# Kernel optimization log

Measured on AMD Instinct MI355X. Metric: run time of the kernel, lower is better.

Reference implementation:

```python
import jax, jax.numpy as jnp
import numpy as np

B, L = 64, 2048
N_RESTYPE, N_GROUP, N_ATOM = 21, 8, 14


def _compose(R1, t1, R2, t2):
    # rigid compose: (R1,t1) o (R2,t2) = (R1@R2, R1@t2 + t1)
    R = jnp.einsum('...ij,...jk->...ik', R1, R2)
    t = jnp.einsum('...ij,...j->...i', R1, t2) + t1
    return R, t


def setup_inputs() -> dict:
    key = jax.random.key(0)
    ks = jax.random.split(key, 8)
    return {
        'bb_rots': jax.random.normal(ks[0], (B, L, 3, 3), jnp.float32),
        'bb_trans': jax.random.normal(ks[1], (B, L, 3), jnp.float32),
        'angles': jax.random.normal(ks[2], (B, L, 7, 2), jnp.float32),
        'aatype': jax.random.randint(ks[3], (B, L), 0, N_RESTYPE),
        'default_frames': jax.random.normal(ks[4], (N_RESTYPE, N_GROUP, 4, 4), jnp.float32),
        'group_idx': jax.random.randint(ks[5], (N_RESTYPE, N_ATOM), 0, N_GROUP),
        'atom_mask': jax.random.uniform(ks[6], (N_RESTYPE, N_ATOM), jnp.float32),
        'lit_positions': jax.random.normal(ks[7], (N_RESTYPE, N_ATOM, 3), jnp.float32),
    }


def reference(bb_rots, bb_trans, angles, aatype, default_frames, group_idx, atom_mask, lit_positions):
    # ---- torsion_angles_to_frames ----
    d4 = default_frames[aatype]                      # [B,L,8,4,4]
    dR, dt = d4[..., :3, :3], d4[..., :3, 3]
    # prepend identity backbone torsion (sin=0, cos=1)
    bb = jnp.broadcast_to(jnp.array([0.0, 1.0], angles.dtype), (*angles.shape[:-2], 1, 2))
    ang = jnp.concatenate([bb, angles], axis=-2)     # [B,L,8,2]
    s, c = ang[..., 0], ang[..., 1]
    z, o = jnp.zeros_like(s), jnp.ones_like(s)
    # rotation about x-axis built from (sin, cos)
    rotx = jnp.stack([
        jnp.stack([o, z, z], axis=-1),
        jnp.stack([z, c, -s], axis=-1),
        jnp.stack([z, s, c], axis=-1),
    ], axis=-2)                                      # [B,L,8,3,3]
    fR = jnp.einsum('blgij,blgjk->blgik', dR, rotx)  # default_r.compose(all_rots)
    ft = dt                                          # all_rots has zero translation
    # chain chi2..chi4 onto chi1
    R5, t5 = _compose(fR[:, :, 4], ft[:, :, 4], fR[:, :, 5], ft[:, :, 5])
    R6, t6 = _compose(R5, t5, fR[:, :, 6], ft[:, :, 6])
    R7, t7 = _compose(R6, t6, fR[:, :, 7], ft[:, :, 7])
    Rbb = jnp.concatenate([fR[:, :, :5], R5[:, :, None], R6[:, :, None], R7[:, :, None]], axis=2)
    tbb = jnp.concatenate([ft[:, :, :5], t5[:, :, None], t6[:, :, None], t7[:, :, None]], axis=2)
    # compose with global backbone frame
    Rg = jnp.einsum('blij,blgjk->blgik', bb_rots, Rbb)          # [B,L,8,3,3]
    tg = jnp.einsum('blij,blgj->blgi', bb_rots, tbb) + bb_trans[:, :, None]

    # ---- frames_and_literature_positions_to_atom14_pos ----
    gidx = group_idx[aatype]                                    # [B,L,14]
    Ra = jnp.take_along_axis(Rg, gidx[:, :, :, None, None], axis=2)  # [B,L,14,3,3]
    ta = jnp.take_along_axis(tg, gidx[:, :, :, None], axis=2)        # [B,L,14,3]
    lit = lit_positions[aatype]                                 # [B,L,14,3]
    mask = atom_mask[aatype][..., None]                         # [B,L,14,1]
    pred = jnp.einsum('blaij,blaj->blai', Ra, lit) + ta
    return pred * mask
```

## Files before the change

kernel.cpp:

```cpp
#include <hip/hip_runtime.h>


constexpr int NRES_TOTAL = 64 * 2048;
constexpr int NRT = 21;
constexpr int NG  = 8;
constexpr int NA  = 14;

__global__ __launch_bounds__(256) void protein_mapper_kernel(
    const float* __restrict__ bb_rots,
    const float* __restrict__ bb_trans,
    const float* __restrict__ angles,
    const int*   __restrict__ aatype,
    const float* __restrict__ default_frames,
    const int*   __restrict__ group_idx,
    const float* __restrict__ atom_mask,
    const float* __restrict__ lit_positions,
    float* __restrict__ out)
{
    __shared__ float s_frames[NRT * NG * 16];
    __shared__ int   s_gidx[NRT * NA];
    __shared__ float s_mask[NRT * NA];
    __shared__ float s_lit[NRT * NA * 3];

    for (int j = threadIdx.x; j < NRT * NG * 16; j += 256) s_frames[j] = default_frames[j];
    for (int j = threadIdx.x; j < NRT * NA; j += 256) {
        s_gidx[j] = group_idx[j];
        s_mask[j] = atom_mask[j];
    }
    for (int j = threadIdx.x; j < NRT * NA * 3; j += 256) s_lit[j] = lit_positions[j];
    __syncthreads();

    const int i = blockIdx.x * 256 + threadIdx.x;
    if (i >= NRES_TOTAL) return;

    const int aa = aatype[i];

    float sv[NG], cv[NG];
    sv[0] = 0.0f; cv[0] = 1.0f;
    const float2* angp = reinterpret_cast<const float2*>(angles + (size_t)i * 14);
    #pragma unroll
    for (int g = 1; g < NG; ++g) {
        float2 sc = angp[g - 1];
        sv[g] = sc.x;
        cv[g] = sc.y;
    }

    float R[NG][9], t[NG][3];
    const float* fr = s_frames + aa * (NG * 16);
    #pragma unroll
    for (int g = 0; g < NG; ++g) {
        const float* m = fr + g * 16;
        const float cg = cv[g], sg = sv[g];
        #pragma unroll
        for (int r = 0; r < 3; ++r) {
            const float a0 = m[r * 4 + 0], a1 = m[r * 4 + 1], a2 = m[r * 4 + 2];
            R[g][r * 3 + 0] = a0;
            R[g][r * 3 + 1] = cg * a1 + sg * a2;
            R[g][r * 3 + 2] = cg * a2 - sg * a1;
            t[g][r] = m[r * 4 + 3];
        }
    }

    #pragma unroll
    for (int g = 5; g < NG; ++g) {
        float Q[9], tq[3];
        #pragma unroll
        for (int r = 0; r < 3; ++r) {
            const float p0 = R[g - 1][r * 3 + 0];
            const float p1 = R[g - 1][r * 3 + 1];
            const float p2 = R[g - 1][r * 3 + 2];
            #pragma unroll
            for (int cdx = 0; cdx < 3; ++cdx)
                Q[r * 3 + cdx] = p0 * R[g][cdx] + p1 * R[g][3 + cdx] + p2 * R[g][6 + cdx];
            tq[r] = p0 * t[g][0] + p1 * t[g][1] + p2 * t[g][2] + t[g - 1][r];
        }
        #pragma unroll
        for (int k = 0; k < 9; ++k) R[g][k] = Q[k];
        t[g][0] = tq[0]; t[g][1] = tq[1]; t[g][2] = tq[2];
    }

    const float* br = bb_rots + (size_t)i * 9;
    const float b00 = br[0], b01 = br[1], b02 = br[2];
    const float b10 = br[3], b11 = br[4], b12 = br[5];
    const float b20 = br[6], b21 = br[7], b22 = br[8];
    const float* btp = bb_trans + (size_t)i * 3;
    const float bt0 = btp[0], bt1 = btp[1], bt2 = btp[2];

    int   ga[NA];
    float mk[NA];
    #pragma unroll
    for (int a = 0; a < NA; ++a) {
        ga[a] = s_gidx[aa * NA + a];
        mk[a] = s_mask[aa * NA + a];
    }

    float res[NA * 3];
    #pragma unroll
    for (int g = 0; g < NG; ++g) {
        #pragma unroll
        for (int a = 0; a < NA; ++a) {
            if (ga[a] == g) {
                const float lx = s_lit[(aa * NA + a) * 3 + 0];
                const float ly = s_lit[(aa * NA + a) * 3 + 1];
                const float lz = s_lit[(aa * NA + a) * 3 + 2];
                const float px = R[g][0] * lx + R[g][1] * ly + R[g][2] * lz + t[g][0];
                const float py = R[g][3] * lx + R[g][4] * ly + R[g][5] * lz + t[g][1];
                const float pz = R[g][6] * lx + R[g][7] * ly + R[g][8] * lz + t[g][2];
                const float qx = b00 * px + b01 * py + b02 * pz + bt0;
                const float qy = b10 * px + b11 * py + b12 * pz + bt1;
                const float qz = b20 * px + b21 * py + b22 * pz + bt2;
                const float m_ = mk[a];
                res[a * 3 + 0] = qx * m_;
                res[a * 3 + 1] = qy * m_;
                res[a * 3 + 2] = qz * m_;
            }
        }
    }

    float2* op2 = reinterpret_cast<float2*>(out + (size_t)i * (NA * 3));
    #pragma unroll
    for (int k = 0; k < (NA * 3) / 2; ++k) {
        float2 v;
        v.x = res[2 * k + 0];
        v.y = res[2 * k + 1];
        op2[k] = v;
    }
}

extern "C" void kernel_launch(void* const* d_in, const int* in_sizes, int n_in,
                              void* d_out, int out_size, void* d_ws, size_t ws_size,
                              hipStream_t stream) {
    const float* bb_rots        = (const float*)d_in[0];
    const float* bb_trans       = (const float*)d_in[1];
    const float* angles         = (const float*)d_in[2];
    const int*   aatype         = (const int*)d_in[3];
    const float* default_frames = (const float*)d_in[4];
    const int*   group_idx      = (const int*)d_in[5];
    const float* atom_mask      = (const float*)d_in[6];
    const float* lit_positions  = (const float*)d_in[7];
    float* out = (float*)d_out;

    const int blocks = (NRES_TOTAL + 255) / 256;
    protein_mapper_kernel<<<blocks, 256, 0, stream>>>(
        bb_rots, bb_trans, angles, aatype,
        default_frames, group_idx, atom_mask, lit_positions, out);
}
```

Baseline: 108.2 us.

## Transpose shared tables by restype and select group frames with branchless muxes

Shared-memory lookup tables are stored transposed (element-major, restype-minor) so that threads with different aatype hit different LDS banks instead of strided rows. The per-atom group selection is replaced by a 3-level binary select tree over the 8 frames, so each atom is computed once instead of through a predicated 8x14 loop. Results are streamed directly into float2 stores per atom pair without a res array. This trades extra select instructions per atom for fewer divergent predicated blocks and less register pressure.

Result: faster. 93.46 us (-13.6%).

```diff
diff --git a/kernel.cpp b/kernel.cpp
--- a/kernel.cpp
+++ b/kernel.cpp
@@ -17,17 +17,24 @@
     const float* __restrict__ lit_positions,
     float* __restrict__ out)
 {
-    __shared__ float s_frames[NRT * NG * 16];
-    __shared__ int   s_gidx[NRT * NA];
-    __shared__ float s_mask[NRT * NA];
-    __shared__ float s_lit[NRT * NA * 3];
+    __shared__ float s_frames[128 * NRT];
+    __shared__ int   s_gidx[NA * NRT];
+    __shared__ float s_mask[NA * NRT];
+    __shared__ float s_lit[NA * 3 * NRT];
 
-    for (int j = threadIdx.x; j < NRT * NG * 16; j += 256) s_frames[j] = default_frames[j];
-    for (int j = threadIdx.x; j < NRT * NA; j += 256) {
-        s_gidx[j] = group_idx[j];
-        s_mask[j] = atom_mask[j];
+    for (int n = threadIdx.x; n < NRT * 128; n += 256) {
+        const int aa = n / 128, j = n % 128;
+        s_frames[j * NRT + aa] = default_frames[n];
     }
-    for (int j = threadIdx.x; j < NRT * NA * 3; j += 256) s_lit[j] = lit_positions[j];
+    for (int n = threadIdx.x; n < NRT * NA; n += 256) {
+        const int aa = n / NA, a = n % NA;
+        s_gidx[a * NRT + aa] = group_idx[n];
+        s_mask[a * NRT + aa] = atom_mask[n];
+    }
+    for (int n = threadIdx.x; n < NRT * NA * 3; n += 256) {
+        const int aa = n / (NA * 3), k = n % (NA * 3);
+        s_lit[k * NRT + aa] = lit_positions[n];
+    }
     __syncthreads();
 
     const int i = blockIdx.x * 256 + threadIdx.x;
@@ -45,38 +52,38 @@
         cv[g] = sc.y;
     }
 
-    float R[NG][9], t[NG][3];
-    const float* fr = s_frames + aa * (NG * 16);
+    float G[NG][12];
     #pragma unroll
     for (int g = 0; g < NG; ++g) {
-        const float* m = fr + g * 16;
         const float cg = cv[g], sg = sv[g];
         #pragma unroll
         for (int r = 0; r < 3; ++r) {
-            const float a0 = m[r * 4 + 0], a1 = m[r * 4 + 1], a2 = m[r * 4 + 2];
-            R[g][r * 3 + 0] = a0;
-            R[g][r * 3 + 1] = cg * a1 + sg * a2;
-            R[g][r * 3 + 2] = cg * a2 - sg * a1;
-            t[g][r] = m[r * 4 + 3];
+            const float a0 = s_frames[(g * 16 + r * 4 + 0) * NRT + aa];
+            const float a1 = s_frames[(g * 16 + r * 4 + 1) * NRT + aa];
+            const float a2 = s_frames[(g * 16 + r * 4 + 2) * NRT + aa];
+            const float a3 = s_frames[(g * 16 + r * 4 + 3) * NRT + aa];
+            G[g][r * 3 + 0] = a0;
+            G[g][r * 3 + 1] = cg * a1 + sg * a2;
+            G[g][r * 3 + 2] = cg * a2 - sg * a1;
+            G[g][9 + r]     = a3;
         }
     }
 
     #pragma unroll
     for (int g = 5; g < NG; ++g) {
-        float Q[9], tq[3];
+        float Q[12];
         #pragma unroll
         for (int r = 0; r < 3; ++r) {
-            const float p0 = R[g - 1][r * 3 + 0];
-            const float p1 = R[g - 1][r * 3 + 1];
-            const float p2 = R[g - 1][r * 3 + 2];
+            const float p0 = G[g - 1][r * 3 + 0];
+            const float p1 = G[g - 1][r * 3 + 1];
+            const float p2 = G[g - 1][r * 3 + 2];
             #pragma unroll
             for (int cdx = 0; cdx < 3; ++cdx)
-                Q[r * 3 + cdx] = p0 * R[g][cdx] + p1 * R[g][3 + cdx] + p2 * R[g][6 + cdx];
-            tq[r] = p0 * t[g][0] + p1 * t[g][1] + p2 * t[g][2] + t[g - 1][r];
+                Q[r * 3 + cdx] = p0 * G[g][cdx] + p1 * G[g][3 + cdx] + p2 * G[g][6 + cdx];
+            Q[9 + r] = p0 * G[g][9] + p1 * G[g][10] + p2 * G[g][11] + G[g - 1][9 + r];
         }
         #pragma unroll
-        for (int k = 0; k < 9; ++k) R[g][k] = Q[k];
-        t[g][0] = tq[0]; t[g][1] = tq[1]; t[g][2] = tq[2];
+        for (int k = 0; k < 12; ++k) G[g][k] = Q[k];
     }
 
     const float* br = bb_rots + (size_t)i * 9;
@@ -86,44 +93,44 @@
     const float* btp = bb_trans + (size_t)i * 3;
     const float bt0 = btp[0], bt1 = btp[1], bt2 = btp[2];
 
-    int   ga[NA];
-    float mk[NA];
-    #pragma unroll
-    for (int a = 0; a < NA; ++a) {
-        ga[a] = s_gidx[aa * NA + a];
-        mk[a] = s_mask[aa * NA + a];
-    }
-
-    float res[NA * 3];
-    #pragma unroll
-    for (int g = 0; g < NG; ++g) {
+    auto atom_pos = [&](int a, float& qx, float& qy, float& qz) {
+        const int   ga = s_gidx[a * NRT + aa];
+        const float m_ = s_mask[a * NRT + aa];
+        const float lx = s_lit[(a * 3 + 0) * NRT + aa];
+        const float ly = s_lit[(a * 3 + 1) * NRT + aa];
+        const float lz = s_lit[(a * 3 + 2) * NRT + aa];
+        const bool b0_ = ga & 1, b1_ = ga & 2, b2_ = ga & 4;
+        float S[12];
         #pragma unroll
-        for (int a = 0; a < NA; ++a) {
-            if (ga[a] == g) {
-                const float lx = s_lit[(aa * NA + a) * 3 + 0];
-                const float ly = s_lit[(aa * NA + a) * 3 + 1];
-                const float lz = s_lit[(aa * NA + a) * 3 + 2];
-                const float px = R[g][0] * lx + R[g][1] * ly + R[g][2] * lz + t[g][0];
-                const float py = R[g][3] * lx + R[g][4] * ly + R[g][5] * lz + t[g][1];
-                const float pz = R[g][6] * lx + R[g][7] * ly + R[g][8] * lz + t[g][2];
-                const float qx = b00 * px + b01 * py + b02 * pz + bt0;
-                const float qy = b10 * px + b11 * py + b12 * pz + bt1;
-                const float qz = b20 * px + b21 * py + b22 * pz + bt2;
-                const float m_ = mk[a];
-                res[a * 3 + 0] = qx * m_;
-                res[a * 3 + 1] = qy * m_;
-                res[a * 3 + 2] = qz * m_;
-            }
+        for (int e = 0; e < 12; ++e) {
+            const float t0 = b0_ ? G[1][e] : G[0][e];
+            const float t1 = b0_ ? G[3][e] : G[2][e];
+            const float t2 = b0_ ? G[5][e] : G[4][e];
+            const float t3 = b0_ ? G[7][e] : G[6][e];
+            const float u0 = b1_ ? t1 : t0;
+            const float u1 = b1_ ? t3 : t2;
+            S[e] = b2_ ? u1 : u0;
         }
-    }
+        const float px = S[0] * lx + S[1] * ly + S[2] * lz + S[9];
+        const float py = S[3] * lx + S[4] * ly + S[5] * lz + S[10];
+        const float pz = S[6] * lx + S[7] * ly + S[8] * lz + S[11];
+        qx = (b00 * px + b01 * py + b02 * pz + bt0) * m_;
+        qy = (b10 * px + b11 * py + b12 * pz + bt1) * m_;
+        qz = (b20 * px + b21 * py + b22 * pz + bt2) * m_;
+    };
 
     float2* op2 = reinterpret_cast<float2*>(out + (size_t)i * (NA * 3));
     #pragma unroll
-    for (int k = 0; k < (NA * 3) / 2; ++k) {
-        float2 v;
-        v.x = res[2 * k + 0];
-        v.y = res[2 * k + 1];
-        op2[k] = v;
+    for (int ap = 0; ap < NA / 2; ++ap) {
+        float qx0, qy0, qz0, qx1, qy1, qz1;
+        atom_pos(2 * ap + 0, qx0, qy0, qz0);
+        atom_pos(2 * ap + 1, qx1, qy1, qz1);
+        float2 v0; v0.x = qx0; v0.y = qy0;
+        float2 v1; v1.x = qz0; v1.y = qx1;
+        float2 v2; v2.x = qy1; v2.y = qz1;
+        op2[3 * ap + 0] = v0;
+        op2[3 * ap + 1] = v1;
+        op2[3 * ap + 2] = v2;
     }
 }
 
```
